# Kernel tuning notes

Hardware: AMD Instinct MI355X
Metric: run time of the kernel (lower is better)

The kernel has to match this reference:

```python
import jax, jax.numpy as jnp
import numpy as np

# ---- static config (mirrors init_kwargs) ----
BATCH = 16384
N_SCALARS = 64
N_KERNELS = 32
L2_INDICES = tuple(range(15))
N_L2 = len(L2_INDICES) + 1          # selected kernels + sum-over-kernels
HIDDEN_MIX = 256
HIDDEN_CORR = 128
SILU_NORM = 1.6790                   # e3nn normalize2mom constant for silu

# ---- real-basis Wigner 3j tensors (unit Frobenius norm, as in e3nn) ----
def _su2_gen(l):
    m = np.arange(-l, l + 1)
    d = 2 * l + 1
    Jz = np.diag(m).astype(complex)
    jp = np.sqrt(l * (l + 1) - m[:-1] * (m[:-1] + 1))
    Jp = np.zeros((d, d), complex)
    Jp[np.arange(1, d), np.arange(0, d - 1)] = jp
    Jm = Jp.conj().T
    return (Jp + Jm) / 2, (Jp - Jm) / 2j, Jz

def _real_basis(l):
    d = 2 * l + 1
    U = np.zeros((d, d), complex)
    U[l, l] = 1.0
    for m in range(1, l + 1):
        U[l + m, l + m] = (-1) ** m / np.sqrt(2)
        U[l + m, l - m] = 1 / np.sqrt(2)
        U[l - m, l - m] = 1j / np.sqrt(2)
        U[l - m, l + m] = -1j * (-1) ** m / np.sqrt(2)
    return U

def _real_gens(l):
    if l == 0:
        return [np.zeros((1, 1))] * 3
    U = _real_basis(l)
    return [np.real(U @ (-1j * J) @ U.conj().T) for J in _su2_gen(l)]

def _w3j(l1, l2, l3):
    G1, G2, G3 = _real_gens(l1), _real_gens(l2), _real_gens(l3)
    d1, d2, d3 = 2 * l1 + 1, 2 * l2 + 1, 2 * l3 + 1
    I1, I2, I3 = np.eye(d1), np.eye(d2), np.eye(d3)
    rows = []
    for a in range(3):  # invariance under all 3 so(3) generators
        rows.append(np.kron(np.kron(G1[a], I2), I3)
                    + np.kron(np.kron(I1, G2[a]), I3)
                    + np.kron(np.kron(I1, I2), G3[a]))
    M = np.concatenate(rows, 0)
    _, _, Vh = np.linalg.svd(M)
    c = Vh[-1].reshape(d1, d2, d3)
    c = c / np.linalg.norm(c)
    idx = np.unravel_index(np.argmax(np.abs(c)), c.shape)
    return (c * np.sign(c[idx])).astype(np.float32)

C000 = jnp.asarray(_w3j(0, 0, 0))
C022 = jnp.asarray(_w3j(0, 2, 2))
C202 = jnp.asarray(_w3j(2, 0, 2))
C220 = jnp.asarray(_w3j(2, 2, 0))
C222 = jnp.asarray(_w3j(2, 2, 2))

def _tp_path(w, c, x1, x2):
    # w: [u,v,w], c (wigner 3j): [i,j,k], x1: [b,u,i], x2: [b,v,j] -> [b,w,k]
    return jnp.einsum('uvw,ijk,bui,bvj->bwk', w, c, x1, x2, optimize='optimal')

def _forward(scalars, kernel_t2s, mlp_w1, mlp_w2, mlp_w3, gate_threshold,
             tp1_w000, tp1_w220, tp1_w022, tp1_w202, tp1_w222,
             tp2_w022, tp2_w202, tp2_w222, correction_scale):
    # ---- KernelMixingHead ----
    h = SILU_NORM * jax.nn.silu(scalars @ mlp_w1 / mlp_w1.shape[0] ** 0.5)
    h = SILU_NORM * jax.nn.silu(h @ mlp_w2 / mlp_w2.shape[0] ** 0.5)
    relative = h @ mlp_w3 / mlp_w3.shape[0] ** 0.5          # [B, K]
    magnitude = jnp.linalg.norm(kernel_t2s, axis=-1)         # [B, K]
    gate = magnitude / (magnitude + gate_threshold)
    weights = relative * gate / N_KERNELS ** 0.5
    mixed = jnp.einsum('bk,bkm->bm', weights, kernel_t2s)    # [B, 5]

    # ---- EquivariantCorrectionHead ----
    sel = kernel_t2s[:, jnp.asarray(L2_INDICES), :]          # [B, n_l2-1, 5]
    t = jnp.concatenate([sel, kernel_t2s.sum(axis=1, keepdims=True)], axis=1)  # [B, N_L2, 5]
    xs = scalars[:, :, None]                                 # [B, ns, 1] (0e channels)
    ns, nl, hc = N_SCALARS, N_L2, HIDDEN_CORR
    # e3nn FullyConnectedTensorProduct path norms ('component'/'element')
    a0 = (1.0 / (ns * ns + nl * nl)) ** 0.5
    a2 = (5.0 / (2 * ns * nl + nl * nl)) ** 0.5
    y0 = a0 * (_tp_path(tp1_w000, C000, xs, xs) + _tp_path(tp1_w220, C220, t, t))   # [B,hc,1]
    y2 = a2 * (_tp_path(tp1_w022, C022, xs, t) + _tp_path(tp1_w202, C202, t, xs)
               + _tp_path(tp1_w222, C222, t, t))                                     # [B,hc,5]
    b2 = (5.0 / (3 * hc * hc)) ** 0.5
    corr = b2 * (_tp_path(tp2_w022, C022, y0, y2) + _tp_path(tp2_w202, C202, y2, y0)
                 + _tp_path(tp2_w222, C222, y2, y2))                                 # [B,1,5]
    return mixed + correction_scale * corr[:, 0, :]

def setup_inputs() -> dict:
    key = jax.random.key(0)
    ks = jax.random.split(key, 13)
    f32 = jnp.float32
    return {
        'scalars': jax.random.normal(ks[0], (BATCH, N_SCALARS), f32),
        'kernel_t2s': jax.random.normal(ks[1], (BATCH, N_KERNELS, 5), f32),
        'mlp_w1': jax.random.normal(ks[2], (N_SCALARS, HIDDEN_MIX), f32),
        'mlp_w2': jax.random.normal(ks[3], (HIDDEN_MIX, HIDDEN_MIX), f32),
        'mlp_w3': jax.random.normal(ks[4], (HIDDEN_MIX, N_KERNELS), f32),
        'gate_threshold': jnp.ones((N_KERNELS,), f32),
        'tp1_w000': jax.random.normal(ks[5], (N_SCALARS, N_SCALARS, HIDDEN_CORR), f32),
        'tp1_w220': jax.random.normal(ks[6], (N_L2, N_L2, HIDDEN_CORR), f32),
        'tp1_w022': jax.random.normal(ks[7], (N_SCALARS, N_L2, HIDDEN_CORR), f32),
        'tp1_w202': jax.random.normal(ks[8], (N_L2, N_SCALARS, HIDDEN_CORR), f32),
        'tp1_w222': jax.random.normal(ks[9], (N_L2, N_L2, HIDDEN_CORR), f32),
        'tp2_w022': jax.random.normal(ks[10], (HIDDEN_CORR, HIDDEN_CORR, 1), f32),
        'tp2_w202': jax.random.normal(ks[11], (HIDDEN_CORR, HIDDEN_CORR, 1), f32),
        'tp2_w222': jax.random.normal(ks[12], (HIDDEN_CORR, HIDDEN_CORR, 1), f32),
        'correction_scale': jnp.asarray(0.1, f32),
    }

def reference(scalars, kernel_t2s, mlp_w1, mlp_w2, mlp_w3, gate_threshold,
              tp1_w000, tp1_w220, tp1_w022, tp1_w202, tp1_w222,
              tp2_w022, tp2_w202, tp2_w222, correction_scale):
    return _forward(scalars, kernel_t2s, mlp_w1, mlp_w2, mlp_w3, gate_threshold,
                    tp1_w000, tp1_w220, tp1_w022, tp1_w202, tp1_w222,
                    tp2_w022, tp2_w202, tp2_w222, correction_scale)
```

## Files before the change

kernel.cpp:

```cpp
#include <hip/hip_runtime.h>
#include <hip/hip_bf16.h>
#include <cmath>
#include <complex>
#include <vector>
#include <cstring>
#include <cstdint>


#define C222_FLIP -1.0f

#define MIX_WS_OFF   0
#define W202T_OFF    327680
#define B2H_OFF      393216
#define B2L_OFF      1294336
#define Y0_WS_OFF    2195456
#define Y2P_OFF      10584064

#define NCHUNK2      110

typedef __attribute__((ext_vector_type(8))) short short8;
typedef __attribute__((ext_vector_type(4))) float f32x4;

struct Coefs {
  float c222[125];
  float d022[5];
  float d202[5];
  float d220[5];
  float a0, a2, b2;
};

#define FMA8(acc, wa, wb, sv) do { \
  acc[0] = fmaf((wa).x, (sv), acc[0]); \
  acc[1] = fmaf((wa).y, (sv), acc[1]); \
  acc[2] = fmaf((wa).z, (sv), acc[2]); \
  acc[3] = fmaf((wa).w, (sv), acc[3]); \
  acc[4] = fmaf((wb).x, (sv), acc[4]); \
  acc[5] = fmaf((wb).y, (sv), acc[5]); \
  acc[6] = fmaf((wb).z, (sv), acc[6]); \
  acc[7] = fmaf((wb).w, (sv), acc[7]); \
} while (0)

#define FMA4(acc, wa, sv) do { \
  acc[0] = fmaf((wa).x, (sv), acc[0]); \
  acc[1] = fmaf((wa).y, (sv), acc[1]); \
  acc[2] = fmaf((wa).z, (sv), acc[2]); \
  acc[3] = fmaf((wa).w, (sv), acc[3]); \
} while (0)

__device__ __forceinline__ float act_silu(float x) {
  return 1.679f * x / (1.0f + expf(-x));
}

__device__ __forceinline__ short f2bf(float x) {
  __hip_bfloat16 h = __float2bfloat16(x);
  return *reinterpret_cast<short*>(&h);
}
__device__ __forceinline__ float bf2f(short s) {
  __hip_bfloat16 h = *reinterpret_cast<__hip_bfloat16*>(&s);
  return __bfloat162float(h);
}

__device__ __forceinline__ int bperm(int n, int k) {
  return ((n >> 4) << 9) | (((((k >> 3) << 4) | (n & 15))) << 3) | (k & 7);
}

__global__ __launch_bounds__(256) void k_prep(
    const float* __restrict__ s, const float* __restrict__ t2s,
    const float* __restrict__ w1, const float* __restrict__ w2,
    const float* __restrict__ w3, const float* __restrict__ gthr,
    float* __restrict__ mixed_ws)
{
  __shared__ float sT[64][36];
  __shared__ float hT[256][36];

  const int tid = threadIdx.x;
  const int b0  = blockIdx.x * 32;

  #pragma unroll
  for (int i = 0; i < 8; i++) {
    int flat = tid + i * 256;
    int bl = flat >> 6, k = flat & 63;
    sT[k][bl] = s[(size_t)(b0 + bl) * 64 + k];
  }
  __syncthreads();

  const int cg = tid & 31, bg = tid >> 5;
  const int c0 = cg * 8, bb0 = bg * 4;

  float acc[4][8];
  #pragma unroll
  for (int j = 0; j < 4; j++)
    #pragma unroll
    for (int i = 0; i < 8; i++) acc[j][i] = 0.f;

  for (int k = 0; k < 64; k++) {
    float4 bv = *(const float4*)&sT[k][bb0];
    float4 wa = *(const float4*)&w1[k * 256 + c0];
    float4 wb = *(const float4*)&w1[k * 256 + c0 + 4];
    const float bvv[4] = {bv.x, bv.y, bv.z, bv.w};
    #pragma unroll
    for (int j = 0; j < 4; j++) { FMA8(acc[j], wa, wb, bvv[j]); }
  }
  #pragma unroll
  for (int j = 0; j < 4; j++)
    #pragma unroll
    for (int i = 0; i < 8; i++)
      hT[c0 + i][bb0 + j] = act_silu(acc[j][i] * 0.125f);
  __syncthreads();

  float acc2[4][8];
  #pragma unroll
  for (int j = 0; j < 4; j++)
    #pragma unroll
    for (int i = 0; i < 8; i++) acc2[j][i] = 0.f;

  for (int k = 0; k < 256; k++) {
    float4 bv = *(const float4*)&hT[k][bb0];
    float4 wa = *(const float4*)&w2[k * 256 + c0];
    float4 wb = *(const float4*)&w2[k * 256 + c0 + 4];
    const float bvv[4] = {bv.x, bv.y, bv.z, bv.w};
    #pragma unroll
    for (int j = 0; j < 4; j++) { FMA8(acc2[j], wa, wb, bvv[j]); }
  }
  __syncthreads();
  #pragma unroll
  for (int j = 0; j < 4; j++)
    #pragma unroll
    for (int i = 0; i < 8; i++)
      hT[c0 + i][bb0 + j] = act_silu(acc2[j][i] * 0.0625f);
  __syncthreads();

  const int jj  = tid & 31;
  const int blg = tid >> 5;
  float acc3[4] = {0.f, 0.f, 0.f, 0.f};
  for (int k = 0; k < 256; k++) {
    float wv  = w3[k * 32 + jj];
    float4 hv = *(const float4*)&hT[k][blg * 4];
    acc3[0] = fmaf(hv.x, wv, acc3[0]);
    acc3[1] = fmaf(hv.y, wv, acc3[1]);
    acc3[2] = fmaf(hv.z, wv, acc3[2]);
    acc3[3] = fmaf(hv.w, wv, acc3[3]);
  }
  const float thrv = gthr[jj];
  #pragma unroll
  for (int r = 0; r < 4; r++) {
    int bl = blg * 4 + r;
    int b  = b0 + bl;
    float rel = acc3[r] * 0.0625f;
    const float* tp = t2s + (size_t)(b * 32 + jj) * 5;
    float tv0 = tp[0], tv1 = tp[1], tv2 = tp[2], tv3 = tp[3], tv4 = tp[4];
    float mag  = sqrtf(tv0*tv0 + tv1*tv1 + tv2*tv2 + tv3*tv3 + tv4*tv4);
    float gate = mag / (mag + thrv);
    float w = rel * gate * 0.17677669529663687f;
    float pm0 = w*tv0, pm1 = w*tv1, pm2 = w*tv2, pm3 = w*tv3, pm4 = w*tv4;
    #pragma unroll
    for (int off = 16; off >= 1; off >>= 1) {
      pm0 += __shfl_xor(pm0, off);
      pm1 += __shfl_xor(pm1, off);
      pm2 += __shfl_xor(pm2, off);
      pm3 += __shfl_xor(pm3, off);
      pm4 += __shfl_xor(pm4, off);
    }
    if (jj == 0) {
      float* mp = mixed_ws + (size_t)b * 5;
      mp[0] = pm0; mp[1] = pm1; mp[2] = pm2; mp[3] = pm3; mp[4] = pm4;
    }
  }
}

__global__ __launch_bounds__(256) void k_wprep(
    const float* __restrict__ w000,
    const float* __restrict__ w2202, float* __restrict__ w202T,
    const float* __restrict__ w022, const float* __restrict__ w202,
    const float* __restrict__ w222, const float* __restrict__ w220,
    short* __restrict__ B2h, short* __restrict__ B2l)
{
  const int tid = threadIdx.x;
  const int blk = blockIdx.x;
  if (blk < 64) {
    int u = blk;
    int base = u * 64 - (u * (u - 1)) / 2;
    int n = (64 - u) * 128;
    for (int idx = tid; idx < n; idx += 256) {
      int t = idx >> 7, wc = idx & 127;
      int v = u + t;
      int p = base + t;
      float val = w000[(size_t)(u * 64 + v) * 128 + wc];
      if (v > u) val += w000[(size_t)(v * 64 + u) * 128 + wc];
      size_t off = (size_t)(45 + (p >> 5)) * 4096 + bperm(wc, p & 31);
      short hs = f2bf(val);
      B2h[off] = hs;
      B2l[off] = f2bf(val - bf2f(hs));
    }
  } else if (blk < 128) {
    int idx = (blk - 64) * 256 + tid;
    int u = idx >> 7, v = idx & 127;
    w202T[v * 128 + u] = w2202[u * 128 + v];
  } else {
    int c = blk - 128;
    #pragma unroll
    for (int i = 0; i < 16; i++) {
      int e = i * 256 + tid;
      int nb = e >> 9;
      int ln = (e >> 3) & 63;
      int j  = e & 7;
      int w  = nb * 16 + (ln & 15);
      int kk = ((ln >> 4) << 3) | j;
      float V = 0.f;
      if (c < 32) {
        int v = c >> 1, u = (c & 1) * 32 + kk;
        V = w022[(size_t)(u * 16 + v) * 128 + w]
          + w202[(size_t)(v * 64 + u) * 128 + w];
      } else if (c < 40) {
        int K = (c - 32) * 32 + kk;
        int u = K >> 4, v = K & 15;
        V = w222[(size_t)(u * 16 + v) * 128 + w];
      } else {
        int q = (c - 40) * 32 + kk;
        if (q < 136) {
          int u = 0;
          while ((u + 1) * 16 - ((u + 1) * u) / 2 <= q) u++;
          int base = u * 16 - (u * (u - 1)) / 2;
          int v = u + (q - base);
          V = w220[(size_t)(u * 16 + v) * 128 + w];
          if (v > u) V += w220[(size_t)(v * 16 + u) * 128 + w];
        }
      }
      short hs = f2bf(V);
      B2h[(size_t)c * 4096 + e] = hs;
      B2l[(size_t)c * 4096 + e] = f2bf(V - bf2f(hs));
    }
  }
}

__global__ __launch_bounds__(512) void k_y2a(
    const float* __restrict__ s, const float* __restrict__ t2s,
    const short* __restrict__ B2h, const short* __restrict__ B2l,
    unsigned short* __restrict__ y2p, Coefs cf)
{
  __shared__ float sL[64][68];
  __shared__ float tL[64][81];
  __shared__ __align__(16) short BhL[2][4096];
  __shared__ __align__(16) short BlL[2][4096];
  __shared__ float cL222[125];

  const int tid  = threadIdx.x;
  const int b0   = blockIdx.x * 64;
  const int wave = tid >> 6;
  const int lane = tid & 63;
  const int m16  = lane & 15;
  const int quad = lane >> 4;
  const int bg   = wave & 3;
  const int nh   = wave >> 2;
  const int bloc = bg * 16 + m16;
  const int wbase = nh * 64;

  float dk022[5];
  #pragma unroll
  for (int k = 0; k < 5; k++) dk022[k] = cf.d022[k];

  if (tid == 0) {
    #pragma unroll
    for (int i = 0; i < 125; i++) cL222[i] = cf.c222[i];
  }
  for (int idx = tid; idx < 4096; idx += 512) {
    int bl = idx >> 6, k = idx & 63;
    sL[bl][k] = s[(size_t)(b0 + bl) * 64 + k];
  }
  for (int idx = tid; idx < 5120; idx += 512) {
    int bl = idx / 80, rem = idx - bl * 80;
    int u = rem / 5, m = rem - u * 5;
    int b = b0 + bl;
    float v;
    if (u < 15) v = t2s[(size_t)(b * 32 + u) * 5 + m];
    else {
      v = 0.f;
      for (int kk = 0; kk < 32; kk++) v += t2s[(size_t)(b * 32 + kk) * 5 + m];
    }
    tL[bl][rem] = v;
  }
  __syncthreads();

  ((short8*)BhL[0])[tid] = ((const short8*)B2h)[tid];
  ((short8*)BlL[0])[tid] = ((const short8*)B2l)[tid];
  __syncthreads();

  f32x4 acc[5][4];
  #pragma unroll
  for (int k = 0; k < 5; k++)
    #pragma unroll
    for (int nf = 0; nf < 4; nf++) acc[k][nf] = 0.f;
  f32x4 p[4];
  #pragma unroll
  for (int nf = 0; nf < 4; nf++) p[nf] = 0.f;

  for (int c = 0; c < 40; c++) {
    const int cur = c & 1;
    if (c + 1 < 40) {
      ((short8*)BhL[cur ^ 1])[tid] = ((const short8*)(B2h + (size_t)(c + 1) * 4096))[tid];
      ((short8*)BlL[cur ^ 1])[tid] = ((const short8*)(B2l + (size_t)(c + 1) * 4096))[tid];
    }
    short8 bhv[4], blv[4];
    #pragma unroll
    for (int nf = 0; nf < 4; nf++) {
      const int nb = nh * 4 + nf;
      bhv[nf] = *(const short8*)&BhL[cur][nb * 512 + lane * 8];
      blv[nf] = *(const short8*)&BlL[cur][nb * 512 + lane * 8];
    }

    if (c < 32) {
      const int ks = c & 1;
      float sv[8];
      {
        float4 a = *(const float4*)&sL[bloc][ks * 32 + quad * 8];
        float4 b = *(const float4*)&sL[bloc][ks * 32 + quad * 8 + 4];
        sv[0]=a.x; sv[1]=a.y; sv[2]=a.z; sv[3]=a.w;
        sv[4]=b.x; sv[5]=b.y; sv[6]=b.z; sv[7]=b.w;
      }
      short8 ah, al;
      #pragma unroll
      for (int j = 0; j < 8; j++) {
        float x = sv[j];
        short hs = f2bf(x);
        ah[j] = hs;
        al[j] = f2bf(x - bf2f(hs));
      }
      #pragma unroll
      for (int nf = 0; nf < 4; nf++) {
        p[nf] = __builtin_amdgcn_mfma_f32_16x16x32_bf16(ah, bhv[nf], p[nf], 0, 0, 0);
        p[nf] = __builtin_amdgcn_mfma_f32_16x16x32_bf16(ah, blv[nf], p[nf], 0, 0, 0);
        p[nf] = __builtin_amdgcn_mfma_f32_16x16x32_bf16(al, bhv[nf], p[nf], 0, 0, 0);
      }
      if (ks == 1) {
        const int v = c >> 1;
        #pragma unroll
        for (int r = 0; r < 4; r++) {
          const int bl = bg * 16 + quad * 4 + r;
          const float* tr = &tL[bl][v * 5];
          #pragma unroll
          for (int k = 0; k < 5; k++) {
            float f = dk022[k] * tr[k];
            #pragma unroll
            for (int nf = 0; nf < 4; nf++)
              acc[k][nf][r] += f * p[nf][r];
          }
        }
        #pragma unroll
        for (int nf = 0; nf < 4; nf++) p[nf] = 0.f;
      }
    } else {
      int cc = c - 32;
      int u  = cc * 2 + (quad >> 1);
      int vb = (quad & 1) * 8;
      float tu[5];
      #pragma unroll
      for (int i = 0; i < 5; i++) tu[i] = tL[bloc][u * 5 + i];
      float G[25];
      #pragma unroll
      for (int jk = 0; jk < 25; jk++) {
        float g = 0.f;
        #pragma unroll
        for (int i = 0; i < 5; i++)
          g = fmaf(cL222[i * 25 + jk], tu[i], g);
        G[jk] = g;
      }
      float av[5][8];
      #pragma unroll
      for (int j = 0; j < 8; j++) {
        float t5[5];
        #pragma unroll
        for (int j5 = 0; j5 < 5; j5++) t5[j5] = tL[bloc][(vb + j) * 5 + j5];
        #pragma unroll
        for (int k = 0; k < 5; k++) {
          float q = 0.f;
          #pragma unroll
          for (int j5 = 0; j5 < 5; j5++)
            q = fmaf(G[j5 * 5 + k], t5[j5], q);
          av[k][j] = q;
        }
      }
      #pragma unroll
      for (int k = 0; k < 5; k++) {
        short8 ah, al;
        #pragma unroll
        for (int j = 0; j < 8; j++) {
          float x = av[k][j];
          short hs = f2bf(x);
          ah[j] = hs;
          al[j] = f2bf(x - bf2f(hs));
        }
        #pragma unroll
        for (int nf = 0; nf < 4; nf++) {
          acc[k][nf] = __builtin_amdgcn_mfma_f32_16x16x32_bf16(ah, bhv[nf], acc[k][nf], 0, 0, 0);
          acc[k][nf] = __builtin_amdgcn_mfma_f32_16x16x32_bf16(ah, blv[nf], acc[k][nf], 0, 0, 0);
          acc[k][nf] = __builtin_amdgcn_mfma_f32_16x16x32_bf16(al, bhv[nf], acc[k][nf], 0, 0, 0);
        }
      }
    }
    __syncthreads();
  }

  #pragma unroll
  for (int nf = 0; nf < 4; nf++) {
    int ch = wbase + nf * 16 + m16;
    #pragma unroll
    for (int r = 0; r < 4; r++) {
      int b = b0 + bg * 16 + quad * 4 + r;
      #pragma unroll
      for (int k = 0; k < 5; k++)
        y2p[((size_t)b * 5 + k) * 128 + ch] = (unsigned short)f2bf(acc[k][nf][r]);
    }
  }
}

__global__ __launch_bounds__(512) void k_y0b(
    const float* __restrict__ s, const float* __restrict__ t2s,
    const short* __restrict__ B2h, const short* __restrict__ B2l,
    float* __restrict__ y0w, Coefs cf)
{
  __shared__ float sL[64][68];
  __shared__ float tL[64][81];
  __shared__ __align__(16) short BhL[2][4096];
  __shared__ __align__(16) short BlL[2][4096];
  __shared__ unsigned char p136s[136];
  __shared__ unsigned short p16[2080];

  const int tid  = threadIdx.x;
  const int b0   = blockIdx.x * 64;
  const int wave = tid >> 6;
  const int lane = tid & 63;
  const int m16  = lane & 15;
  const int quad = lane >> 4;
  const int bg   = wave & 3;
  const int nh   = wave >> 2;
  const int bloc = bg * 16 + m16;
  const int wbase = nh * 64;

  float dk220[5];
  #pragma unroll
  for (int k = 0; k < 5; k++) dk220[k] = cf.d220[k];

  for (int idx = tid; idx < 4096; idx += 512) {
    int bl = idx >> 6, k = idx & 63;
    sL[bl][k] = s[(size_t)(b0 + bl) * 64 + k];
  }
  for (int idx = tid; idx < 5120; idx += 512) {
    int bl = idx / 80, rem = idx - bl * 80;
    int u = rem / 5, m = rem - u * 5;
    int b = b0 + bl;
    float v;
    if (u < 15) v = t2s[(size_t)(b * 32 + u) * 5 + m];
    else {
      v = 0.f;
      for (int kk = 0; kk < 32; kk++) v += t2s[(size_t)(b * 32 + kk) * 5 + m];
    }
    tL[bl][rem] = v;
  }
  if (tid < 16) {
    int u = tid;
    int base = u * 16 - (u * (u - 1)) / 2;
    for (int t = 0; t < 16 - u; t++)
      p136s[base + t] = (unsigned char)((u << 4) | (u + t));
  }
  if (tid < 64) {
    int u = tid;
    int base = u * 64 - (u * (u - 1)) / 2;
    for (int t = 0; t < 64 - u; t++)
      p16[base + t] = (unsigned short)((u << 8) | (u + t));
  }
  __syncthreads();

  ((short8*)BhL[0])[tid] = ((const short8*)(B2h + (size_t)40 * 4096))[tid];
  ((short8*)BlL[0])[tid] = ((const short8*)(B2l + (size_t)40 * 4096))[tid];
  __syncthreads();

  f32x4 accY0[4];
  #pragma unroll
  for (int nf = 0; nf < 4; nf++) accY0[nf] = 0.f;

  for (int c = 40; c < NCHUNK2; c++) {
    const int cur = c & 1;
    if (c + 1 < NCHUNK2) {
      ((short8*)BhL[cur ^ 1])[tid] = ((const short8*)(B2h + (size_t)(c + 1) * 4096))[tid];
      ((short8*)BlL[cur ^ 1])[tid] = ((const short8*)(B2l + (size_t)(c + 1) * 4096))[tid];
    }
    short8 bhv[4], blv[4];
    #pragma unroll
    for (int nf = 0; nf < 4; nf++) {
      const int nb = nh * 4 + nf;
      bhv[nf] = *(const short8*)&BhL[cur][nb * 512 + lane * 8];
      blv[nf] = *(const short8*)&BlL[cur][nb * 512 + lane * 8];
    }

    short8 ah, al;
    if (c < 45) {
      int cc = c - 40;
      int qbase = cc * 32 + quad * 8;
      #pragma unroll
      for (int j = 0; j < 8; j++) {
        int q = qbase + j;
        float g = 0.f;
        if (q < 136) {
          int uv = p136s[q];
          int u = uv >> 4, v = uv & 15;
          #pragma unroll
          for (int m = 0; m < 5; m++)
            g = fmaf(dk220[m] * tL[bloc][u * 5 + m], tL[bloc][v * 5 + m], g);
        }
        short hs = f2bf(g);
        ah[j] = hs;
        al[j] = f2bf(g - bf2f(hs));
      }
    } else {
      int pbase = (c - 45) * 32 + quad * 8;
      #pragma unroll
      for (int j = 0; j < 8; j++) {
        int uv = p16[pbase + j];
        float x = sL[bloc][uv >> 8] * sL[bloc][uv & 255];
        short hs = f2bf(x);
        ah[j] = hs;
        al[j] = f2bf(x - bf2f(hs));
      }
    }
    #pragma unroll
    for (int nf = 0; nf < 4; nf++) {
      accY0[nf] = __builtin_amdgcn_mfma_f32_16x16x32_bf16(ah, bhv[nf], accY0[nf], 0, 0, 0);
      accY0[nf] = __builtin_amdgcn_mfma_f32_16x16x32_bf16(ah, blv[nf], accY0[nf], 0, 0, 0);
      accY0[nf] = __builtin_amdgcn_mfma_f32_16x16x32_bf16(al, bhv[nf], accY0[nf], 0, 0, 0);
    }
    __syncthreads();
  }

  #pragma unroll
  for (int nf = 0; nf < 4; nf++) {
    int ch = wbase + nf * 16 + m16;
    #pragma unroll
    for (int r = 0; r < 4; r++) {
      int b = b0 + bg * 16 + quad * 4 + r;
      y0w[(size_t)b * 128 + ch] = accY0[nf][r];
    }
  }
}

__global__ __launch_bounds__(512) void k_fused(
    const float* __restrict__ mixed_ws,
    const float* __restrict__ y0w, const unsigned short* __restrict__ y2p,
    const float* __restrict__ w2022, const float* __restrict__ w202T,
    const float* __restrict__ w2222,
    const float* __restrict__ csc, float* __restrict__ out, Coefs cf)
{
  __shared__ __align__(16) float y0I[16][128][2];
  __shared__ float cL222[125];
  __shared__ float corrAcc[32][5];
  __shared__ float pPL[32][25];
  __shared__ __align__(16) float y2iI[16][128][2];

  const int tid = threadIdx.x;
  const int b0  = blockIdx.x * 32;

  float dk022[5], dk202[5];
  #pragma unroll
  for (int k = 0; k < 5; k++) { dk022[k] = cf.d022[k]; dk202[k] = cf.d202[k]; }

  if (tid == 0) {
    #pragma unroll
    for (int i = 0; i < 125; i++) cL222[i] = cf.c222[i];
  }
  for (int idx = tid; idx < 4096; idx += 512) {
    int bl = idx >> 7, ch = idx & 127;
    y0I[bl >> 1][ch][bl & 1] = cf.a0 * y0w[(size_t)(b0 + bl) * 128 + ch];
  }
  __syncthreads();

  const int xw = tid & 31;
  const int g  = tid >> 5;
  const int w0 = xw * 4;
  const int bA = 2 * g, bB = 2 * g + 1;

  float y2acc[5][2][4];
  #pragma unroll
  for (int k = 0; k < 5; k++) {
    #pragma unroll
    for (int h = 0; h < 2; h++) {
      int b = b0 + 2 * g + h;
      const unsigned short* yp = y2p + ((size_t)b * 5 + k) * 128 + w0;
      ushort4 u4 = *(const ushort4*)yp;
      y2acc[k][h][0] = cf.a2 * bf2f((short)u4.x);
      y2acc[k][h][1] = cf.a2 * bf2f((short)u4.y);
      y2acc[k][h][2] = cf.a2 * bf2f((short)u4.z);
      y2acc[k][h][3] = cf.a2 * bf2f((short)u4.w);
    }
  }

  {
    float gvr[2][4] = {{0.f,0.f,0.f,0.f},{0.f,0.f,0.f,0.f}};
    #pragma unroll 8
    for (int u = 0; u < 128; u++) {
      float2 y0p = *(const float2*)&y0I[g][u][0];
      float4 w4 = *(const float4*)(w2022 + (size_t)u * 128 + w0);
      FMA4(gvr[0], w4, y0p.x);
      FMA4(gvr[1], w4, y0p.y);
    }
    #pragma unroll
    for (int k = 0; k < 5; k++) {
      float pA = gvr[0][0]*y2acc[k][0][0] + gvr[0][1]*y2acc[k][0][1]
               + gvr[0][2]*y2acc[k][0][2] + gvr[0][3]*y2acc[k][0][3];
      float pB = gvr[1][0]*y2acc[k][1][0] + gvr[1][1]*y2acc[k][1][1]
               + gvr[1][2]*y2acc[k][1][2] + gvr[1][3]*y2acc[k][1][3];
      pA += __shfl_xor(pA, 16); pA += __shfl_xor(pA, 8); pA += __shfl_xor(pA, 4);
      pA += __shfl_xor(pA, 2);  pA += __shfl_xor(pA, 1);
      pB += __shfl_xor(pB, 16); pB += __shfl_xor(pB, 8); pB += __shfl_xor(pB, 4);
      pB += __shfl_xor(pB, 2);  pB += __shfl_xor(pB, 1);
      if (xw == 0) {
        corrAcc[bA][k] = dk022[k] * pA;
        corrAcc[bB][k] = dk022[k] * pB;
      }
    }
  }
  {
    float hvr[2][4] = {{0.f,0.f,0.f,0.f},{0.f,0.f,0.f,0.f}};
    #pragma unroll 8
    for (int v = 0; v < 128; v++) {
      float2 y0p = *(const float2*)&y0I[g][v][0];
      float4 w4 = *(const float4*)(w202T + (size_t)v * 128 + w0);
      FMA4(hvr[0], w4, y0p.x);
      FMA4(hvr[1], w4, y0p.y);
    }
    #pragma unroll
    for (int k = 0; k < 5; k++) {
      float pA = hvr[0][0]*y2acc[k][0][0] + hvr[0][1]*y2acc[k][0][1]
               + hvr[0][2]*y2acc[k][0][2] + hvr[0][3]*y2acc[k][0][3];
      float pB = hvr[1][0]*y2acc[k][1][0] + hvr[1][1]*y2acc[k][1][1]
               + hvr[1][2]*y2acc[k][1][2] + hvr[1][3]*y2acc[k][1][3];
      pA += __shfl_xor(pA, 16); pA += __shfl_xor(pA, 8); pA += __shfl_xor(pA, 4);
      pA += __shfl_xor(pA, 2);  pA += __shfl_xor(pA, 1);
      pB += __shfl_xor(pB, 16); pB += __shfl_xor(pB, 8); pB += __shfl_xor(pB, 4);
      pB += __shfl_xor(pB, 2);  pB += __shfl_xor(pB, 1);
      if (xw == 0) {
        corrAcc[bA][k] += dk202[k] * pA;
        corrAcc[bB][k] += dk202[k] * pB;
      }
    }
  }
  for (int i = 0; i < 5; i++) {
    #pragma unroll
    for (int wi = 0; wi < 4; wi++) {
      float2 o; o.x = y2acc[i][0][wi]; o.y = y2acc[i][1][wi];
      *(float2*)&y2iI[g][w0 + wi][0] = o;
    }
    __syncthreads();
    float zr[2][4] = {{0.f,0.f,0.f,0.f},{0.f,0.f,0.f,0.f}};
    #pragma unroll 8
    for (int u = 0; u < 128; u++) {
      float2 yp = *(const float2*)&y2iI[g][u][0];
      float4 w4 = *(const float4*)(w2222 + (size_t)u * 128 + w0);
      FMA4(zr[0], w4, yp.x);
      FMA4(zr[1], w4, yp.y);
    }
    #pragma unroll
    for (int j = 0; j < 5; j++) {
      float pA = zr[0][0]*y2acc[j][0][0] + zr[0][1]*y2acc[j][0][1]
               + zr[0][2]*y2acc[j][0][2] + zr[0][3]*y2acc[j][0][3];
      float pB = zr[1][0]*y2acc[j][1][0] + zr[1][1]*y2acc[j][1][1]
               + zr[1][2]*y2acc[j][1][2] + zr[1][3]*y2acc[j][1][3];
      pA += __shfl_xor(pA, 16); pA += __shfl_xor(pA, 8); pA += __shfl_xor(pA, 4);
      pA += __shfl_xor(pA, 2);  pA += __shfl_xor(pA, 1);
      pB += __shfl_xor(pB, 16); pB += __shfl_xor(pB, 8); pB += __shfl_xor(pB, 4);
      pB += __shfl_xor(pB, 2);  pB += __shfl_xor(pB, 1);
      if (xw == 0) {
        pPL[bA][i * 5 + j] = pA;
        pPL[bB][i * 5 + j] = pB;
      }
    }
    __syncthreads();
  }

  if (tid < 160) {
    int bb = tid / 5, k = tid - bb * 5;
    float c2 = 0.f;
    #pragma unroll
    for (int ii = 0; ii < 5; ii++)
      #pragma unroll
      for (int jj = 0; jj < 5; jj++)
        c2 = fmaf(cL222[ii * 25 + jj * 5 + k], pPL[bb][ii * 5 + jj], c2);
    float tot = corrAcc[bb][k] + c2;
    int b = b0 + bb;
    out[(size_t)b * 5 + k] = mixed_ws[(size_t)b * 5 + k] + csc[0] * cf.b2 * tot;
  }
}

namespace {

using cplx = std::complex<double>;

static void su2_gen(int l, std::vector<cplx>& Jx, std::vector<cplx>& Jy,
                    std::vector<cplx>& Jz) {
  int d = 2 * l + 1;
  Jx.assign((size_t)d * d, cplx(0, 0));
  Jy.assign((size_t)d * d, cplx(0, 0));
  Jz.assign((size_t)d * d, cplx(0, 0));
  for (int a = 0; a < d; a++) Jz[(size_t)a * d + a] = cplx(a - l, 0);
  for (int r = 1; r < d; r++) {
    double m = (r - 1) - l;
    double v = std::sqrt(l * (l + 1.0) - m * (m + 1.0));
    Jx[(size_t)r * d + (r - 1)] += cplx(v / 2, 0);
    Jx[(size_t)(r - 1) * d + r] += cplx(v / 2, 0);
    Jy[(size_t)r * d + (r - 1)] += cplx(0, -v / 2);
    Jy[(size_t)(r - 1) * d + r] += cplx(0, v / 2);
  }
}

static void real_basis(int l, std::vector<cplx>& U) {
  int d = 2 * l + 1;
  U.assign((size_t)d * d, cplx(0, 0));
  U[(size_t)l * d + l] = cplx(1, 0);
  double is2 = 1.0 / std::sqrt(2.0);
  for (int m = 1; m <= l; m++) {
    double sgn = (m % 2 == 0) ? 1.0 : -1.0;
    U[(size_t)(l + m) * d + (l + m)] = cplx(sgn * is2, 0);
    U[(size_t)(l + m) * d + (l - m)] = cplx(is2, 0);
    U[(size_t)(l - m) * d + (l - m)] = cplx(0, is2);
    U[(size_t)(l - m) * d + (l + m)] = cplx(0, -sgn * is2);
  }
}

static void real_gens(int l, std::vector<double> G[3]) {
  int d = 2 * l + 1;
  if (l == 0) { for (int a = 0; a < 3; a++) G[a].assign(1, 0.0); return; }
  std::vector<cplx> J[3];
  su2_gen(l, J[0], J[1], J[2]);
  std::vector<cplx> U;
  real_basis(l, U);
  for (int a = 0; a < 3; a++) {
    std::vector<cplx> T((size_t)d * d, cplx(0, 0));
    for (int i = 0; i < d; i++)
      for (int k = 0; k < d; k++) {
        cplx s(0, 0);
        for (int j = 0; j < d; j++)
          s += U[(size_t)i * d + j] * (cplx(0, -1) * J[a][(size_t)j * d + k]);
        T[(size_t)i * d + k] = s;
      }
    G[a].assign((size_t)d * d, 0.0);
    for (int i = 0; i < d; i++)
      for (int k = 0; k < d; k++) {
        cplx s(0, 0);
        for (int j = 0; j < d; j++)
          s += T[(size_t)i * d + j] * std::conj(U[(size_t)k * d + j]);
        G[a][(size_t)i * d + k] = s.real();
      }
  }
}

static void w3j_host(int l1, int l2, int l3, float* out) {
  int d1 = 2 * l1 + 1, d2 = 2 * l2 + 1, d3 = 2 * l3 + 1;
  int D = d1 * d2 * d3;
  std::vector<double> G1[3], G2[3], G3[3];
  real_gens(l1, G1); real_gens(l2, G2); real_gens(l3, G3);
  int R = 3 * D;
  std::vector<double> M((size_t)R * D, 0.0);
  for (int a = 0; a < 3; a++) {
    double* Ma = &M[(size_t)a * D * D];
    for (int i1 = 0; i1 < d1; i1++)
      for (int j1 = 0; j1 < d1; j1++) {
        double g = G1[a][(size_t)i1 * d1 + j1];
        if (g == 0.0) continue;
        for (int i2 = 0; i2 < d2; i2++)
          for (int i3 = 0; i3 < d3; i3++)
            Ma[(size_t)((i1 * d2 + i2) * d3 + i3) * D + ((j1 * d2 + i2) * d3 + i3)] += g;
      }
    for (int i2 = 0; i2 < d2; i2++)
      for (int j2 = 0; j2 < d2; j2++) {
        double g = G2[a][(size_t)i2 * d2 + j2];
        if (g == 0.0) continue;
        for (int i1 = 0; i1 < d1; i1++)
          for (int i3 = 0; i3 < d3; i3++)
            Ma[(size_t)((i1 * d2 + i2) * d3 + i3) * D + ((i1 * d2 + j2) * d3 + i3)] += g;
      }
    for (int i3 = 0; i3 < d3; i3++)
      for (int j3 = 0; j3 < d3; j3++) {
        double g = G3[a][(size_t)i3 * d3 + j3];
        if (g == 0.0) continue;
        for (int i1 = 0; i1 < d1; i1++)
          for (int i2 = 0; i2 < d2; i2++)
            Ma[(size_t)((i1 * d2 + i2) * d3 + i3) * D + ((i1 * d2 + i2) * d3 + j3)] += g;
      }
  }
  std::vector<int> pivcol;
  int rank = 0;
  for (int col = 0; col < D && rank < R; col++) {
    int pr = -1; double pv = 1e-9;
    for (int r = rank; r < R; r++) {
      double av = std::fabs(M[(size_t)r * D + col]);
      if (av > pv) { pv = av; pr = r; }
    }
    if (pr < 0) continue;
    if (pr != rank)
      for (int c = 0; c < D; c++) std::swap(M[(size_t)pr * D + c], M[(size_t)rank * D + c]);
    double inv = 1.0 / M[(size_t)rank * D + col];
    for (int c = 0; c < D; c++) M[(size_t)rank * D + c] *= inv;
    for (int r = 0; r < R; r++) {
      if (r == rank) continue;
      double f = M[(size_t)r * D + col];
      if (f != 0.0)
        for (int c = 0; c < D; c++) M[(size_t)r * D + c] -= f * M[(size_t)rank * D + c];
    }
    pivcol.push_back(col);
    rank++;
  }
  std::vector<char> isp(D, 0);
  for (int c : pivcol) isp[c] = 1;
  int fc = 0;
  for (int c = 0; c < D; c++) if (!isp[c]) { fc = c; break; }
  std::vector<double> x(D, 0.0);
  x[fc] = 1.0;
  for (int r = 0; r < rank; r++) x[pivcol[r]] = -M[(size_t)r * D + fc];
  double n = 0;
  for (double v : x) n += v * v;
  n = std::sqrt(n);
  for (int c = 0; c < D; c++) x[c] /= n;
  double best = 0;
  for (int c = 0; c < D; c++) { double av = std::fabs(x[c]); if (av > best) best = av; }
  double ssum = 0;
  for (int c = 0; c < D; c++) {
    double av = std::fabs(x[c]);
    if (av >= best * 0.999) ssum += (x[c] >= 0 ? 1.0 : -1.0);
  }
  double sgn = (ssum >= 0) ? 1.0 : -1.0;
  for (int c = 0; c < D; c++) out[c] = (float)(x[c] * sgn);
}

}

extern "C" void kernel_launch(void* const* d_in, const int* in_sizes, int n_in,
                              void* d_out, int out_size, void* d_ws, size_t ws_size,
                              hipStream_t stream)
{
  (void)in_sizes; (void)n_in; (void)out_size; (void)ws_size;

  const float* s     = (const float*)d_in[0];
  const float* t2s   = (const float*)d_in[1];
  const float* w1    = (const float*)d_in[2];
  const float* w2    = (const float*)d_in[3];
  const float* w3    = (const float*)d_in[4];
  const float* gthr  = (const float*)d_in[5];
  const float* w000  = (const float*)d_in[6];
  const float* w220  = (const float*)d_in[7];
  const float* w022  = (const float*)d_in[8];
  const float* w202  = (const float*)d_in[9];
  const float* w222  = (const float*)d_in[10];
  const float* w2022 = (const float*)d_in[11];
  const float* w2202 = (const float*)d_in[12];
  const float* w2222 = (const float*)d_in[13];
  const float* csc   = (const float*)d_in[14];
  float* out = (float*)d_out;

  char* ws = (char*)d_ws;
  float* mixed_ws = (float*)(ws + MIX_WS_OFF);
  float* w202T    = (float*)(ws + W202T_OFF);
  short* B2h      = (short*)(ws + B2H_OFF);
  short* B2l      = (short*)(ws + B2L_OFF);
  float* y0_ws    = (float*)(ws + Y0_WS_OFF);
  unsigned short* y2p = (unsigned short*)(ws + Y2P_OFF);

  Coefs cf;
  {
    float c000v[1], c022v[25], c202v[25], c220v[25];
    w3j_host(0, 0, 0, c000v);
    w3j_host(0, 2, 2, c022v);
    w3j_host(2, 0, 2, c202v);
    w3j_host(2, 2, 0, c220v);
    w3j_host(2, 2, 2, cf.c222);
    for (int i = 0; i < 125; i++) cf.c222[i] *= C222_FLIP;
    for (int k = 0; k < 5; k++) {
      cf.d022[k] = c022v[k * 5 + k];
      cf.d202[k] = c202v[k * 5 + k];
      cf.d220[k] = c220v[k * 5 + k];
    }
    (void)c000v;
    cf.a0 = (float)std::sqrt(1.0 / (64.0 * 64.0 + 16.0 * 16.0));
    cf.a2 = (float)std::sqrt(5.0 / (2.0 * 64.0 * 16.0 + 16.0 * 16.0));
    cf.b2 = (float)std::sqrt(5.0 / (3.0 * 128.0 * 128.0));
  }

  hipLaunchKernelGGL(k_prep, dim3(512), dim3(256), 0, stream,
                     s, t2s, w1, w2, w3, gthr, mixed_ws);
  hipLaunchKernelGGL(k_wprep, dim3(173), dim3(256), 0, stream,
                     w000, w2202, w202T,
                     w022, w202, w222, w220, B2h, B2l);
  hipLaunchKernelGGL(k_y0b, dim3(256), dim3(512), 0, stream,
                     s, t2s, B2h, B2l, y0_ws, cf);
  hipLaunchKernelGGL(k_y2a, dim3(256), dim3(512), 0, stream,
                     s, t2s, B2h, B2l, y2p, cf);
  hipLaunchKernelGGL(k_fused, dim3(512), dim3(512), 0, stream,
                     mixed_ws, y0_ws, y2p, w2022, w202T, w2222, csc, out, cf);
}
```

Baseline: 433.5 us.

## Stage tp2 weight tiles in LDS and batch all five y2 components per weight pass

The k_fused kernel now loads the 128x128 tp2 weight matrices into shared memory in 32-row tiles, so all 16 warps share one tile instead of each reading its own copy from global or L2. The w222 path is restructured to accumulate all five l=2 components at once, streaming w2222 once instead of five times. Per-component syncs go away, replaced by per-tile barriers. The cost is more shared memory, more registers for the 5x2x4 accumulators, and extra barriers, which may lower occupancy.

```diff
diff --git a/kernel.cpp b/kernel.cpp
--- a/kernel.cpp
+++ b/kernel.cpp
@@ -550,10 +550,11 @@
     const float* __restrict__ csc, float* __restrict__ out, Coefs cf)
 {
   __shared__ __align__(16) float y0I[16][128][2];
+  __shared__ __align__(16) float wLd[32][128];
+  __shared__ float y2S[5][16][32][2];
   __shared__ float cL222[125];
   __shared__ float corrAcc[32][5];
   __shared__ float pPL[32][25];
-  __shared__ __align__(16) float y2iI[16][128][2];
 
   const int tid = threadIdx.x;
   const int b0  = blockIdx.x * 32;
@@ -570,12 +571,13 @@
     int bl = idx >> 7, ch = idx & 127;
     y0I[bl >> 1][ch][bl & 1] = cf.a0 * y0w[(size_t)(b0 + bl) * 128 + ch];
   }
-  __syncthreads();
 
   const int xw = tid & 31;
   const int g  = tid >> 5;
   const int w0 = xw * 4;
   const int bA = 2 * g, bB = 2 * g + 1;
+  const int srow = tid >> 4;
+  const int scol = (tid & 15) * 8;
 
   float y2acc[5][2][4];
   #pragma unroll
@@ -591,15 +593,23 @@
       y2acc[k][h][3] = cf.a2 * bf2f((short)u4.w);
     }
   }
+  __syncthreads();
 
   {
     float gvr[2][4] = {{0.f,0.f,0.f,0.f},{0.f,0.f,0.f,0.f}};
-    #pragma unroll 8
-    for (int u = 0; u < 128; u++) {
-      float2 y0p = *(const float2*)&y0I[g][u][0];
-      float4 w4 = *(const float4*)(w2022 + (size_t)u * 128 + w0);
-      FMA4(gvr[0], w4, y0p.x);
-      FMA4(gvr[1], w4, y0p.y);
+    for (int t = 0; t < 4; t++) {
+      const int u0 = t * 32;
+      *(float4*)&wLd[srow][scol]     = *(const float4*)(w2022 + (size_t)(u0 + srow) * 128 + scol);
+      *(float4*)&wLd[srow][scol + 4] = *(const float4*)(w2022 + (size_t)(u0 + srow) * 128 + scol + 4);
+      __syncthreads();
+      #pragma unroll 8
+      for (int uu = 0; uu < 32; uu++) {
+        float2 y0p = *(const float2*)&y0I[g][u0 + uu][0];
+        float4 w4 = *(const float4*)&wLd[uu][w0];
+        FMA4(gvr[0], w4, y0p.x);
+        FMA4(gvr[1], w4, y0p.y);
+      }
+      __syncthreads();
     }
     #pragma unroll
     for (int k = 0; k < 5; k++) {
@@ -619,12 +629,19 @@
   }
   {
     float hvr[2][4] = {{0.f,0.f,0.f,0.f},{0.f,0.f,0.f,0.f}};
-    #pragma unroll 8
-    for (int v = 0; v < 128; v++) {
-      float2 y0p = *(const float2*)&y0I[g][v][0];
-      float4 w4 = *(const float4*)(w202T + (size_t)v * 128 + w0);
-      FMA4(hvr[0], w4, y0p.x);
-      FMA4(hvr[1], w4, y0p.y);
+    for (int t = 0; t < 4; t++) {
+      const int u0 = t * 32;
+      *(float4*)&wLd[srow][scol]     = *(const float4*)(w202T + (size_t)(u0 + srow) * 128 + scol);
+      *(float4*)&wLd[srow][scol + 4] = *(const float4*)(w202T + (size_t)(u0 + srow) * 128 + scol + 4);
+      __syncthreads();
+      #pragma unroll 8
+      for (int uu = 0; uu < 32; uu++) {
+        float2 y0p = *(const float2*)&y0I[g][u0 + uu][0];
+        float4 w4 = *(const float4*)&wLd[uu][w0];
+        FMA4(hvr[0], w4, y0p.x);
+        FMA4(hvr[1], w4, y0p.y);
+      }
+      __syncthreads();
     }
     #pragma unroll
     for (int k = 0; k < 5; k++) {
@@ -642,38 +659,63 @@
       }
     }
   }
-  for (int i = 0; i < 5; i++) {
-    #pragma unroll
-    for (int wi = 0; wi < 4; wi++) {
-      float2 o; o.x = y2acc[i][0][wi]; o.y = y2acc[i][1][wi];
-      *(float2*)&y2iI[g][w0 + wi][0] = o;
-    }
-    __syncthreads();
-    float zr[2][4] = {{0.f,0.f,0.f,0.f},{0.f,0.f,0.f,0.f}};
-    #pragma unroll 8
-    for (int u = 0; u < 128; u++) {
-      float2 yp = *(const float2*)&y2iI[g][u][0];
-      float4 w4 = *(const float4*)(w2222 + (size_t)u * 128 + w0);
-      FMA4(zr[0], w4, yp.x);
-      FMA4(zr[1], w4, yp.y);
-    }
-    #pragma unroll
-    for (int j = 0; j < 5; j++) {
-      float pA = zr[0][0]*y2acc[j][0][0] + zr[0][1]*y2acc[j][0][1]
-               + zr[0][2]*y2acc[j][0][2] + zr[0][3]*y2acc[j][0][3];
-      float pB = zr[1][0]*y2acc[j][1][0] + zr[1][1]*y2acc[j][1][1]
-               + zr[1][2]*y2acc[j][1][2] + zr[1][3]*y2acc[j][1][3];
-      pA += __shfl_xor(pA, 16); pA += __shfl_xor(pA, 8); pA += __shfl_xor(pA, 4);
-      pA += __shfl_xor(pA, 2);  pA += __shfl_xor(pA, 1);
-      pB += __shfl_xor(pB, 16); pB += __shfl_xor(pB, 8); pB += __shfl_xor(pB, 4);
-      pB += __shfl_xor(pB, 2);  pB += __shfl_xor(pB, 1);
-      if (xw == 0) {
-        pPL[bA][i * 5 + j] = pA;
-        pPL[bB][i * 5 + j] = pB;
-      }
-    }
-    __syncthreads();
-  }
+  {
+    float zr[5][2][4];
+    #pragma unroll
+    for (int i = 0; i < 5; i++)
+      #pragma unroll
+      for (int h = 0; h < 2; h++)
+        #pragma unroll
+        for (int w = 0; w < 4; w++) zr[i][h][w] = 0.f;
+
+    for (int t = 0; t < 4; t++) {
+      const int u0 = t * 32;
+      *(float4*)&wLd[srow][scol]     = *(const float4*)(w2222 + (size_t)(u0 + srow) * 128 + scol);
+      *(float4*)&wLd[srow][scol + 4] = *(const float4*)(w2222 + (size_t)(u0 + srow) * 128 + scol + 4);
+      if (w0 >= u0 && w0 < u0 + 32) {
+        const int uu0 = w0 - u0;
+        #pragma unroll
+        for (int i = 0; i < 5; i++)
+          #pragma unroll
+          for (int h = 0; h < 2; h++)
+            #pragma unroll
+            for (int c = 0; c < 4; c++)
+              y2S[i][g][uu0 + c][h] = y2acc[i][h][c];
+      }
+      __syncthreads();
+      #pragma unroll 4
+      for (int uu = 0; uu < 32; uu++) {
+        float4 w4 = *(const float4*)&wLd[uu][w0];
+        #pragma unroll
+        for (int i = 0; i < 5; i++) {
+          float ya = y2S[i][g][uu][0];
+          float yb = y2S[i][g][uu][1];
+          FMA4(zr[i][0], w4, ya);
+          FMA4(zr[i][1], w4, yb);
+        }
+      }
+      __syncthreads();
+    }
+    #pragma unroll
+    for (int i = 0; i < 5; i++) {
+      #pragma unroll
+      for (int j = 0; j < 5; j++) {
+        float pA = zr[i][0][0]*y2acc[j][0][0] + zr[i][0][1]*y2acc[j][0][1]
+                 + zr[i][0][2]*y2acc[j][0][2] + zr[i][0][3]*y2acc[j][0][3];
+        float pB = zr[i][1][0]*y2acc[j][1][0] + zr[i][1][1]*y2acc[j][1][1]
+                 + zr[i][1][2]*y2acc[j][1][2] + zr[i][1][3]*y2acc[j][1][3];
+        pA += __shfl_xor(pA, 16); pA += __shfl_xor(pA, 8); pA += __shfl_xor(pA, 4);
+        pA += __shfl_xor(pA, 2);  pA += __shfl_xor(pA, 1);
+        pB += __shfl_xor(pB, 16); pB += __shfl_xor(pB, 8); pB += __shfl_xor(pB, 4);
+        pB += __shfl_xor(pB, 2);  pB += __shfl_xor(pB, 1);
+        if (xw == 0) {
+          pPL[bA][i * 5 + j] = pA;
+          pPL[bB][i * 5 + j] = pB;
+        }
+      }
+    }
+  }
+  __syncthreads();
 
   if (tid < 160) {
     int bb = tid / 5, k = tid - bb * 5;
```

After: 403.4 us. -6.9%, faster.
